# Kernel tuning notes

Hardware: AMD Instinct MI355X
Metric: run time of the kernel (lower is better)

The kernel has to match this reference:

```python
import jax, jax.numpy as jnp
import numpy as np

H = 16      # numHeads (== numKeyValueHeads since keyValueHeadsPerHead=1)
D = 128     # headDim


def setup_inputs() -> dict:
    key = jax.random.key(0)
    k1, k2, k3 = jax.random.split(key, 3)
    B, S, dim = 2, 2048, 2048
    x = jax.random.normal(k1, (B, S, dim), dtype=jnp.float32)
    # qkvProj: Linear(dim -> (H + 2*H)*D) without bias; torch Linear weight is [out, in]
    Wqkv = jax.random.normal(k2, ((H + 2 * H) * D, dim), dtype=jnp.float32) * 0.02
    # outProj: Linear(H*D -> dim) without bias
    Wout = jax.random.normal(k3, (dim, H * D), dtype=jnp.float32) * 0.02
    return {"x": x, "Wqkv": Wqkv, "Wout": Wout}


def reference(x, Wqkv, Wout):
    B, S, _ = x.shape
    qkv = jnp.einsum('bsd,ed->bse', x, Wqkv)           # [B, S, 3*H*D]
    qkv = qkv.reshape(B, S, 3 * H, D)
    q = qkv[:, :, :H]                                  # [B, S, H, D]
    k = qkv[:, :, H:2 * H]                             # [B, S, H, D]
    v = qkv[:, :, 2 * H:]                              # [B, S, H, D]
    # explicit QK^T / sqrt(d), softmax in fp32, then @ V (keyValueHeadsPerHead=1
    # collapses the group axis, leaving standard per-head attention)
    logits = jnp.einsum('bqhd,bkhd->bhqk', q, k) * (D ** -0.5)
    w = jax.nn.softmax(logits.astype(jnp.float32), axis=-1).astype(logits.dtype)
    out = jnp.einsum('bhqk,bkhd->bqhd', w, v).reshape(B, S, H * D)
    return jnp.einsum('bse,de->bsd', out, Wout)        # outProj
```

## Files before the change

kernel.cpp:

```cpp
#include <hip/hip_runtime.h>

typedef __bf16 bf16x8 __attribute__((ext_vector_type(8)));
typedef _Float16 f16;
typedef f16 f16x8 __attribute__((ext_vector_type(8)));
typedef float f32x4 __attribute__((ext_vector_type(4)));
typedef unsigned short u16;
typedef u16 u16x4 __attribute__((ext_vector_type(4)));

__device__ __forceinline__ u16 f2bf(float f) {
  unsigned u = __builtin_bit_cast(unsigned, f);
  u += 0x7FFFu + ((u >> 16) & 1u);
  return (u16)(u >> 16);
}

#define GLDS16(g, l) __builtin_amdgcn_global_load_lds(                     \
    (const __attribute__((address_space(1))) unsigned int*)(g),            \
    (__attribute__((address_space(3))) unsigned int*)(l), 16, 0, 0)

__device__ __forceinline__ f32x4 mfma16(bf16x8 a, bf16x8 b, f32x4 c) {
  return __builtin_amdgcn_mfma_f32_16x16x32_bf16(a, b, c, 0, 0, 0);
}
__device__ __forceinline__ f32x4 mfma16h(f16x8 a, f16x8 b, f32x4 c) {
  return __builtin_amdgcn_mfma_f32_16x16x32_f16(a, b, c, 0, 0, 0);
}

__global__ void cvt_bf16(const float* __restrict__ src, u16* __restrict__ dst,
                         int n4, int n4s, float scale) {
  int idx = blockIdx.x * blockDim.x + threadIdx.x;
  int stride = gridDim.x * blockDim.x;
  for (int i = idx; i < n4; i += stride) {
    float4 v = ((const float4*)src)[i];
    float sc = (i < n4s) ? scale : 1.0f;
    u16x4 o = { f2bf(v.x * sc), f2bf(v.y * sc), f2bf(v.z * sc), f2bf(v.w * sc) };
    ((u16x4*)dst)[i] = o;
  }
}

__global__ __launch_bounds__(512, 1) void gemm1_qkv(
    const u16* __restrict__ A, const u16* __restrict__ B,
    u16* __restrict__ QK, u16* __restrict__ VT) {
  __shared__ __align__(16) u16 LA[2][16384];
  __shared__ __align__(16) u16 LB[2][16384];
  constexpr int K = 2048;
  const int t = threadIdx.x, lane = t & 63, w = t >> 6;
  const int wm = w >> 2, wn = w & 3;
  const int l15 = lane & 15, lg = lane >> 4;
  const int l7 = l15 & 7;

  const int bid = blockIdx.x;
  const int wg = (bid & 7) * 48 + (bid >> 3);
  const int bx = wg % 24, by = wg / 24;
  const int m0 = by * 256, n0 = bx * 256;

  const int srow = t >> 3;
  const int schunk = (t & 7) ^ (srow & 7);
  const u16* ga = A + (size_t)(m0 + srow) * K + schunk * 8;
  const u16* gb = B + (size_t)(n0 + srow) * K + schunk * 8;

  f32x4 acc[8][4] = {};

#define STG_A(ch, kt, bfi)                                                 \
    GLDS16(ga + (kt) * 64 + (size_t)(ch) * 64 * K, &LA[bfi][(ch) * 4096] + t * 8)
#define STG_B(ch, kt, bfi)                                                 \
    GLDS16(gb + (kt) * 64 + (size_t)(ch) * 64 * K, &LB[bfi][(ch) * 4096] + t * 8)

  STG_A(0, 0, 0); STG_A(2, 0, 0);
  STG_B(0, 0, 0); STG_B(1, 0, 0); STG_B(2, 0, 0); STG_B(3, 0, 0);
  STG_A(1, 0, 0); STG_A(3, 0, 0);
  asm volatile("s_waitcnt vmcnt(2)" ::: "memory");
  __builtin_amdgcn_s_barrier();

#pragma unroll 1
  for (int T = 0; T < 32; ++T) {
    const int p = T & 1, np = p ^ 1;
    const bool st = (T < 31);
    const u16* la = &LA[p][0];
    const u16* lb = &LB[p][0];
    bf16x8 aF[2][4], bF0[2][2], bF1[2][2];

#pragma unroll
    for (int kk = 0; kk < 2; ++kk) {
      const int cp = ((kk * 4 + lg) ^ l7) * 8;
#pragma unroll
      for (int i = 0; i < 4; ++i)
        aF[kk][i] = *(const bf16x8*)&la[(wm * 128 + i * 16 + l15) * 64 + cp];
#pragma unroll
      for (int j = 0; j < 2; ++j)
        bF0[kk][j] = *(const bf16x8*)&lb[(wn * 64 + j * 16 + l15) * 64 + cp];
    }
    if (st) { STG_A(0, T + 1, np); STG_A(2, T + 1, np); }
    __builtin_amdgcn_s_barrier();
    asm volatile("s_waitcnt lgkmcnt(0)" ::: "memory");
    __builtin_amdgcn_sched_barrier(0);
    __builtin_amdgcn_s_setprio(1);
#pragma unroll
    for (int i = 0; i < 4; ++i)
#pragma unroll
      for (int j = 0; j < 2; ++j)
#pragma unroll
        for (int kk = 0; kk < 2; ++kk)
          acc[i][j] = mfma16(aF[kk][i], bF0[kk][j], acc[i][j]);
    __builtin_amdgcn_s_setprio(0);
    __builtin_amdgcn_s_barrier();

#pragma unroll
    for (int kk = 0; kk < 2; ++kk) {
      const int cp = ((kk * 4 + lg) ^ l7) * 8;
#pragma unroll
      for (int j = 0; j < 2; ++j)
        bF1[kk][j] = *(const bf16x8*)&lb[(wn * 64 + 32 + j * 16 + l15) * 64 + cp];
    }
    if (st) {
      STG_B(0, T + 1, np); STG_B(1, T + 1, np);
      asm volatile("s_waitcnt vmcnt(4)" ::: "memory");
    } else {
      asm volatile("s_waitcnt vmcnt(0)" ::: "memory");
    }
    __builtin_amdgcn_s_barrier();
    asm volatile("s_waitcnt lgkmcnt(0)" ::: "memory");
    __builtin_amdgcn_sched_barrier(0);
    __builtin_amdgcn_s_setprio(1);
#pragma unroll
    for (int i = 0; i < 4; ++i)
#pragma unroll
      for (int j = 0; j < 2; ++j)
#pragma unroll
        for (int kk = 0; kk < 2; ++kk)
          acc[i][2 + j] = mfma16(aF[kk][i], bF1[kk][j], acc[i][2 + j]);
    __builtin_amdgcn_s_setprio(0);
    __builtin_amdgcn_s_barrier();

#pragma unroll
    for (int kk = 0; kk < 2; ++kk) {
      const int cp = ((kk * 4 + lg) ^ l7) * 8;
#pragma unroll
      for (int i = 0; i < 4; ++i)
        aF[kk][i] = *(const bf16x8*)&la[(wm * 128 + 64 + i * 16 + l15) * 64 + cp];
    }
    if (st) { STG_B(2, T + 1, np); STG_B(3, T + 1, np); }
    __builtin_amdgcn_s_barrier();
    asm volatile("s_waitcnt lgkmcnt(0)" ::: "memory");
    __builtin_amdgcn_sched_barrier(0);
    __builtin_amdgcn_s_setprio(1);
#pragma unroll
    for (int i = 0; i < 4; ++i)
#pragma unroll
      for (int j = 0; j < 2; ++j)
#pragma unroll
        for (int kk = 0; kk < 2; ++kk)
          acc[4 + i][j] = mfma16(aF[kk][i], bF0[kk][j], acc[4 + i][j]);
    __builtin_amdgcn_s_setprio(0);
    __builtin_amdgcn_s_barrier();

    if (st) {
      STG_A(1, T + 1, np); STG_A(3, T + 1, np);
      asm volatile("s_waitcnt vmcnt(2)" ::: "memory");
    }
    __builtin_amdgcn_s_barrier();
    __builtin_amdgcn_s_setprio(1);
#pragma unroll
    for (int i = 0; i < 4; ++i)
#pragma unroll
      for (int j = 0; j < 2; ++j)
#pragma unroll
        for (int kk = 0; kk < 2; ++kk)
          acc[4 + i][2 + j] = mfma16(aF[kk][i], bF1[kk][j], acc[4 + i][2 + j]);
    __builtin_amdgcn_s_setprio(0);
    __builtin_amdgcn_s_barrier();
  }
#undef STG_A
#undef STG_B

  const int rb = m0 + wm * 128 + lg * 4;
  const int cb0 = wn * 64 + l15;
  if (n0 < 4096) {
#pragma unroll
    for (int i = 0; i < 8; ++i)
#pragma unroll
      for (int j = 0; j < 4; ++j) {
        const int row0 = rb + i * 16;
        const int col = n0 + cb0 + j * 16;
#pragma unroll
        for (int jj = 0; jj < 4; ++jj)
          QK[(size_t)(row0 + jj) * 4096 + col] = f2bf(acc[i][j][jj]);
      }
  } else {
#pragma unroll
    for (int i = 0; i < 8; ++i)
#pragma unroll
      for (int j = 0; j < 4; ++j) {
        const int row0 = rb + i * 16;
        const int vcol = (n0 - 4096) + cb0 + j * 16;
        const int bb = row0 >> 11, s = row0 & 2047;
        auto h0 = __builtin_amdgcn_cvt_pkrtz(acc[i][j][0], acc[i][j][1]);
        auto h1 = __builtin_amdgcn_cvt_pkrtz(acc[i][j][2], acc[i][j][3]);
        uint2 pk;
        pk.x = __builtin_bit_cast(unsigned, h0);
        pk.y = __builtin_bit_cast(unsigned, h1);
        *(uint2*)&VT[((size_t)bb * 2048 + vcol) * 2048 + s] = pk;
      }
  }
}

__global__ __launch_bounds__(256, 3) void gemm_bt(
    const u16* __restrict__ A, const u16* __restrict__ B,
    float* __restrict__ C, int M, int N, int K) {
  __shared__ __align__(16) u16 As[2][128 * 32];
  __shared__ __align__(16) u16 Bs[2][128 * 32];
  const int t = threadIdx.x;
  const int lane = t & 63;
  const int w = t >> 6;
  const int wm = w >> 1, wn = w & 1;
  const int l15 = lane & 15, lg = lane >> 4;
  const int m0 = blockIdx.y * 128, n0 = blockIdx.x * 128;
  f32x4 acc[4][4] = {};

  const int srow = t >> 2;
  const int schunk = (t & 3) ^ ((srow >> 1) & 3);
  const u16* ga = A + (size_t)(m0 + srow) * K + schunk * 8;
  const u16* gb = B + (size_t)(n0 + srow) * K + schunk * 8;
  const size_t half = (size_t)64 * K;
  const int ro = l15 * 32 + ((lg ^ ((l15 >> 1) & 3)) * 8);

#define STG(kt, bf) do {                                                   \
    const int ko_ = (kt) * 32;                                             \
    GLDS16(ga + ko_,        &As[bf][0] + t * 8);                           \
    GLDS16(ga + half + ko_, &As[bf][2048] + t * 8);                        \
    GLDS16(gb + ko_,        &Bs[bf][0] + t * 8);                           \
    GLDS16(gb + half + ko_, &Bs[bf][2048] + t * 8);                        \
  } while (0)

#define BODY(bf) do {                                                      \
    const u16* la_ = &As[bf][0];                                           \
    const u16* lb_ = &Bs[bf][0];                                           \
    bf16x8 af[4], bfr[4];                                                  \
    _Pragma("unroll")                                                      \
    for (int i_ = 0; i_ < 4; ++i_)                                         \
      af[i_] = *(const bf16x8*)&la_[(wm * 64 + i_ * 16) * 32 + ro];        \
    _Pragma("unroll")                                                      \
    for (int i_ = 0; i_ < 4; ++i_)                                         \
      bfr[i_] = *(const bf16x8*)&lb_[(wn * 64 + i_ * 16) * 32 + ro];       \
    __builtin_amdgcn_s_setprio(1);                                         \
    _Pragma("unroll")                                                      \
    for (int i_ = 0; i_ < 4; ++i_)                                         \
      _Pragma("unroll")                                                    \
      for (int j_ = 0; j_ < 4; ++j_)                                       \
        acc[i_][j_] = mfma16(af[i_], bfr[j_], acc[i_][j_]);                \
    __builtin_amdgcn_s_setprio(0);                                         \
  } while (0)

  const int NT = K / 32;
  STG(0, 0);
#pragma unroll 1
  for (int T = 0; T < NT - 1; ++T) {
    STG(T + 1, (T + 1) & 1);
    asm volatile("s_waitcnt vmcnt(4)" ::: "memory");
    __builtin_amdgcn_sched_barrier(0);
    __builtin_amdgcn_s_barrier();
    __builtin_amdgcn_sched_barrier(0);
    BODY(T & 1);
    asm volatile("s_waitcnt lgkmcnt(0)" ::: "memory");
    __builtin_amdgcn_sched_barrier(0);
    __builtin_amdgcn_s_barrier();
    __builtin_amdgcn_sched_barrier(0);
  }
  asm volatile("s_waitcnt vmcnt(0)" ::: "memory");
  __builtin_amdgcn_sched_barrier(0);
  __builtin_amdgcn_s_barrier();
  __builtin_amdgcn_sched_barrier(0);
  BODY((NT - 1) & 1);
#undef STG
#undef BODY

  const int rbase = m0 + wm * 64 + (lg << 2);
  const int cbase = n0 + wn * 64 + l15;
#pragma unroll
  for (int i = 0; i < 4; ++i)
#pragma unroll
    for (int j = 0; j < 4; ++j) {
      const int row0 = rbase + i * 16;
      const int col = cbase + j * 16;
#pragma unroll
      for (int jj = 0; jj < 4; ++jj)
        C[(size_t)(row0 + jj) * N + col] = acc[i][j][jj];
    }
}

#define PSTRIDE 72
__global__ __launch_bounds__(512, 1) void attn_fwd(
    const u16* __restrict__ qk, const u16* __restrict__ vt, u16* __restrict__ aout) {
  __shared__ __align__(16) u16 Ks[2][64 * 128];
  __shared__ __align__(16) u16 Vs[2][128 * 64];
  __shared__ __align__(16) u16 Pl[8][32 * PSTRIDE];
  const int t = threadIdx.x, lane = t & 63, w = t >> 6;
  const int bh = blockIdx.x;
  const int b = bh >> 4, h = bh & 15;
  const int q0 = blockIdx.y * 256 + w * 32;
  const int l15 = lane & 15, lg = lane >> 4;

  const u16* qp = qk + (size_t)b * 2048 * 4096 + h * 128;
  const u16* kp = qp + 2048;
  const u16* vtp = vt + (size_t)(b * 16 + h) * 128 * 2048;
  u16* op = aout + (size_t)b * 2048 * 2048 + h * 128;

  int ksoff[2], vsoff[2];
#pragma unroll
  for (int rd = 0; rd < 2; ++rd) {
    const int r = rd * 32 + (t >> 4);
    const int c = (t & 15) ^ (r & 15);
    ksoff[rd] = r * 4096 + c * 8;
    const int rv = rd * 64 + (t >> 3);
    const int cv = (t & 7) ^ (rv & 7);
    vsoff[rd] = rv * 2048 + cv * 8;
  }

  bf16x8 qf[2][4];
#pragma unroll
  for (int mi = 0; mi < 2; ++mi)
#pragma unroll
    for (int kd = 0; kd < 4; ++kd)
      qf[mi][kd] = *(const bf16x8*)&qp[(size_t)(q0 + mi * 16 + l15) * 4096 + kd * 32 + lg * 8];

  f32x4 o[2][8] = {};
  f32x4 lacc[2] = {};
  const f16x8 onesf = {f16(1.f), f16(1.f), f16(1.f), f16(1.f),
                       f16(1.f), f16(1.f), f16(1.f), f16(1.f)};
  u16* pw = &Pl[w][0];

#pragma unroll
  for (int rd = 0; rd < 2; ++rd) {
    GLDS16(kp + ksoff[rd], &Ks[0][0] + rd * 4096 + t * 8);
    GLDS16(vtp + vsoff[rd], &Vs[0][0] + rd * 4096 + t * 8);
  }
  __syncthreads();

  auto tile = [&](const u16* ksb, const u16* vsb, u16* kpre, u16* vpre, int nextit) {
    if (nextit < 32) {
      const size_t kt1 = (size_t)nextit * 64;
#pragma unroll
      for (int rd = 0; rd < 2; ++rd) {
        GLDS16(kp + kt1 * 4096 + ksoff[rd], kpre + rd * 4096 + t * 8);
        GLDS16(vtp + kt1 + vsoff[rd], vpre + rd * 4096 + t * 8);
      }
    }
    f32x4 sf[2][4];
    __builtin_amdgcn_s_setprio(1);
#pragma unroll
    for (int ni = 0; ni < 4; ++ni) {
      const int r = ni * 16 + l15;
      bf16x8 kf[4];
#pragma unroll
      for (int kd = 0; kd < 4; ++kd)
        kf[kd] = *(const bf16x8*)&ksb[r * 128 + (((kd * 4 + lg) ^ l15) * 8)];
#pragma unroll
      for (int mi = 0; mi < 2; ++mi) {
        f32x4 s = {0.f, 0.f, 0.f, 0.f};
        s = mfma16(kf[0], qf[mi][0], s);
        s = mfma16(kf[1], qf[mi][1], s);
        s = mfma16(kf[2], qf[mi][2], s);
        s = mfma16(kf[3], qf[mi][3], s);
        sf[mi][ni] = s;
      }
    }
    __builtin_amdgcn_s_setprio(0);

#pragma unroll
    for (int mi = 0; mi < 2; ++mi)
#pragma unroll
      for (int ni = 0; ni < 4; ++ni) {
        float p0 = exp2f(sf[mi][ni][0]);
        float p1 = exp2f(sf[mi][ni][1]);
        float p2 = exp2f(sf[mi][ni][2]);
        float p3 = exp2f(sf[mi][ni][3]);
        auto h0 = __builtin_amdgcn_cvt_pkrtz(p0, p1);
        auto h1 = __builtin_amdgcn_cvt_pkrtz(p2, p3);
        uint2 wv;
        wv.x = __builtin_bit_cast(unsigned, h0);
        wv.y = __builtin_bit_cast(unsigned, h1);
        *(uint2*)&pw[(mi * 16 + l15) * PSTRIDE + ni * 16 + lg * 4] = wv;
      }

    f16x8 pa[2][2];
#pragma unroll
    for (int mi = 0; mi < 2; ++mi)
#pragma unroll
      for (int ks = 0; ks < 2; ++ks)
        pa[mi][ks] = *(const f16x8*)&pw[(mi * 16 + l15) * PSTRIDE + ks * 32 + lg * 8];
    __builtin_amdgcn_s_setprio(1);
#pragma unroll
    for (int mi = 0; mi < 2; ++mi) {
      lacc[mi] = mfma16h(pa[mi][0], onesf, lacc[mi]);
      lacc[mi] = mfma16h(pa[mi][1], onesf, lacc[mi]);
    }
#pragma unroll
    for (int n2 = 0; n2 < 8; ++n2) {
      const int r = n2 * 16 + l15;
      f16x8 vf0 = *(const f16x8*)&vsb[r * 64 + (((0 * 4 + lg) ^ (l15 & 7)) * 8)];
      f16x8 vf1 = *(const f16x8*)&vsb[r * 64 + (((1 * 4 + lg) ^ (l15 & 7)) * 8)];
#pragma unroll
      for (int mi = 0; mi < 2; ++mi) {
        o[mi][n2] = mfma16h(pa[mi][0], vf0, o[mi][n2]);
        o[mi][n2] = mfma16h(pa[mi][1], vf1, o[mi][n2]);
      }
    }
    __builtin_amdgcn_s_setprio(0);
    __syncthreads();
  };

#pragma unroll 1
  for (int it = 0; it < 32; it += 2) {
    tile(&Ks[0][0], &Vs[0][0], &Ks[1][0], &Vs[1][0], it + 1);
    tile(&Ks[1][0], &Vs[1][0], &Ks[0][0], &Vs[0][0], it + 2);
  }

#pragma unroll
  for (int mi = 0; mi < 2; ++mi)
#pragma unroll
    for (int j = 0; j < 4; ++j) {
      float inv = 1.f / lacc[mi][j];
#pragma unroll
      for (int n2 = 0; n2 < 8; ++n2)
        op[(size_t)(q0 + mi * 16 + lg * 4 + j) * 2048 + n2 * 16 + l15] =
            f2bf(o[mi][n2][j] * inv);
    }
}

extern "C" void kernel_launch(void* const* d_in, const int* in_sizes, int n_in,
                              void* d_out, int out_size, void* d_ws, size_t ws_size,
                              hipStream_t stream) {
  const float* x    = (const float*)d_in[0];
  const float* Wqkv = (const float*)d_in[1];
  const float* Wout = (const float*)d_in[2];
  float* out = (float*)d_out;

  u16* ws = (u16*)d_ws;
  u16* xb    = ws;
  u16* wqkvb = ws + 8388608;
  u16* woutb = ws + 20971520;
  u16* qkbuf = ws + 25165824;
  u16* vtbuf = ws + 41943040;
  u16* aout  = xb;

  const float qscale = 0.08838834764831845f * 1.4426950408889634f;

  cvt_bf16<<<2048, 256, 0, stream>>>(x,    xb,    8388608 / 4, 0, 1.0f);
  cvt_bf16<<<2048, 256, 0, stream>>>(Wqkv, wqkvb, 12582912 / 4, 4194304 / 4, qscale);
  cvt_bf16<<<1024, 256, 0, stream>>>(Wout, woutb, 4194304 / 4, 0, 1.0f);

  gemm1_qkv<<<384, 512, 0, stream>>>(xb, wqkvb, qkbuf, vtbuf);
  attn_fwd<<<dim3(32, 8, 1), 512, 0, stream>>>(qkbuf, vtbuf, aout);
  gemm_bt<<<dim3(16, 32), 256, 0, stream>>>(aout, woutb, out, 4096, 2048, 2048);
}
```

Measured before the change: 272.2 us.

## Retile QKV GEMM to 128x192 blocks with two workgroups per CU

The QKV projection GEMM moves from 256x256 tiles with 512 threads, one block per CU and 384 blocks, to 128x192 tiles with 256 threads, two blocks per CU and 1024 blocks. The staging schedule, vmcnt waits and epilogue are reworked so a single tile can span both the QK and V column regions. The intent is better wave quantization across CUs and latency hiding through two resident blocks. The cost is lower data reuse per tile and more global/LDS traffic per FLOP.

```diff
diff --git a/kernel.cpp b/kernel.cpp
--- a/kernel.cpp
+++ b/kernel.cpp
@@ -36,38 +36,39 @@
   }
 }
 
-__global__ __launch_bounds__(512, 1) void gemm1_qkv(
+__global__ __launch_bounds__(256, 2) void gemm1_qkv(
     const u16* __restrict__ A, const u16* __restrict__ B,
     u16* __restrict__ QK, u16* __restrict__ VT) {
-  __shared__ __align__(16) u16 LA[2][16384];
-  __shared__ __align__(16) u16 LB[2][16384];
+  __shared__ __align__(16) u16 LA[2][8192];
+  __shared__ __align__(16) u16 LB[2][12288];
   constexpr int K = 2048;
   const int t = threadIdx.x, lane = t & 63, w = t >> 6;
-  const int wm = w >> 2, wn = w & 3;
+  const int wm = w >> 1, wn = w & 1;
   const int l15 = lane & 15, lg = lane >> 4;
   const int l7 = l15 & 7;
 
   const int bid = blockIdx.x;
-  const int wg = (bid & 7) * 48 + (bid >> 3);
-  const int bx = wg % 24, by = wg / 24;
-  const int m0 = by * 256, n0 = bx * 256;
+  const int wg = (bid & 7) * 128 + (bid >> 3);
+  const int bx = wg & 31, by = wg >> 5;
+  const int m0 = by * 128, n0 = bx * 192;
 
   const int srow = t >> 3;
   const int schunk = (t & 7) ^ (srow & 7);
   const u16* ga = A + (size_t)(m0 + srow) * K + schunk * 8;
   const u16* gb = B + (size_t)(n0 + srow) * K + schunk * 8;
 
-  f32x4 acc[8][4] = {};
+  f32x4 acc[4][6] = {};
 
 #define STG_A(ch, kt, bfi)                                                 \
-    GLDS16(ga + (kt) * 64 + (size_t)(ch) * 64 * K, &LA[bfi][(ch) * 4096] + t * 8)
+    GLDS16(ga + (kt) * 64 + (size_t)(ch) * 32 * K, &LA[bfi][(ch) * 2048] + t * 8)
 #define STG_B(ch, kt, bfi)                                                 \
-    GLDS16(gb + (kt) * 64 + (size_t)(ch) * 64 * K, &LB[bfi][(ch) * 4096] + t * 8)
-
-  STG_A(0, 0, 0); STG_A(2, 0, 0);
-  STG_B(0, 0, 0); STG_B(1, 0, 0); STG_B(2, 0, 0); STG_B(3, 0, 0);
+    GLDS16(gb + (kt) * 64 + (size_t)(ch) * 32 * K, &LB[bfi][(ch) * 2048] + t * 8)
+
+  STG_A(0, 0, 0); STG_A(2, 0, 0); STG_B(0, 0, 0);
+  STG_B(1, 0, 0); STG_B(3, 0, 0); STG_B(4, 0, 0);
+  STG_B(2, 0, 0); STG_B(5, 0, 0);
   STG_A(1, 0, 0); STG_A(3, 0, 0);
-  asm volatile("s_waitcnt vmcnt(2)" ::: "memory");
+  asm volatile("s_waitcnt vmcnt(4)" ::: "memory");
   __builtin_amdgcn_s_barrier();
 
 #pragma unroll 1
@@ -76,30 +77,35 @@
     const bool st = (T < 31);
     const u16* la = &LA[p][0];
     const u16* lb = &LB[p][0];
-    bf16x8 aF[2][4], bF0[2][2], bF1[2][2];
+    bf16x8 aF[2][2], bLo[2][3], bHi[2][3];
 
 #pragma unroll
     for (int kk = 0; kk < 2; ++kk) {
       const int cp = ((kk * 4 + lg) ^ l7) * 8;
 #pragma unroll
-      for (int i = 0; i < 4; ++i)
-        aF[kk][i] = *(const bf16x8*)&la[(wm * 128 + i * 16 + l15) * 64 + cp];
-#pragma unroll
-      for (int j = 0; j < 2; ++j)
-        bF0[kk][j] = *(const bf16x8*)&lb[(wn * 64 + j * 16 + l15) * 64 + cp];
-    }
-    if (st) { STG_A(0, T + 1, np); STG_A(2, T + 1, np); }
+      for (int i = 0; i < 2; ++i)
+        aF[kk][i] = *(const bf16x8*)&la[(wm * 64 + i * 16 + l15) * 64 + cp];
+#pragma unroll
+      for (int j = 0; j < 3; ++j)
+        bLo[kk][j] = *(const bf16x8*)&lb[(wn * 96 + j * 16 + l15) * 64 + cp];
+    }
+    if (st) {
+      STG_A(0, T + 1, np); STG_A(2, T + 1, np); STG_B(0, T + 1, np);
+      asm volatile("s_waitcnt vmcnt(5)" ::: "memory");
+    } else {
+      asm volatile("s_waitcnt vmcnt(2)" ::: "memory");
+    }
     __builtin_amdgcn_s_barrier();
     asm volatile("s_waitcnt lgkmcnt(0)" ::: "memory");
     __builtin_amdgcn_sched_barrier(0);
     __builtin_amdgcn_s_setprio(1);
 #pragma unroll
-    for (int i = 0; i < 4; ++i)
-#pragma unroll
-      for (int j = 0; j < 2; ++j)
+    for (int i = 0; i < 2; ++i)
+#pragma unroll
+      for (int j = 0; j < 3; ++j)
 #pragma unroll
         for (int kk = 0; kk < 2; ++kk)
-          acc[i][j] = mfma16(aF[kk][i], bF0[kk][j], acc[i][j]);
+          acc[i][j] = mfma16(aF[kk][i], bLo[kk][j], acc[i][j]);
     __builtin_amdgcn_s_setprio(0);
     __builtin_amdgcn_s_barrier();
 
@@ -107,12 +113,12 @@
     for (int kk = 0; kk < 2; ++kk) {
       const int cp = ((kk * 4 + lg) ^ l7) * 8;
 #pragma unroll
-      for (int j = 0; j < 2; ++j)
-        bF1[kk][j] = *(const bf16x8*)&lb[(wn * 64 + 32 + j * 16 + l15) * 64 + cp];
+      for (int j = 0; j < 3; ++j)
+        bHi[kk][j] = *(const bf16x8*)&lb[(wn * 96 + 48 + j * 16 + l15) * 64 + cp];
     }
     if (st) {
-      STG_B(0, T + 1, np); STG_B(1, T + 1, np);
-      asm volatile("s_waitcnt vmcnt(4)" ::: "memory");
+      STG_B(1, T + 1, np); STG_B(3, T + 1, np); STG_B(4, T + 1, np);
+      asm volatile("s_waitcnt vmcnt(6)" ::: "memory");
     } else {
       asm volatile("s_waitcnt vmcnt(0)" ::: "memory");
     }
@@ -121,12 +127,12 @@
     __builtin_amdgcn_sched_barrier(0);
     __builtin_amdgcn_s_setprio(1);
 #pragma unroll
-    for (int i = 0; i < 4; ++i)
-#pragma unroll
-      for (int j = 0; j < 2; ++j)
+    for (int i = 0; i < 2; ++i)
+#pragma unroll
+      for (int j = 0; j < 3; ++j)
 #pragma unroll
         for (int kk = 0; kk < 2; ++kk)
-          acc[i][2 + j] = mfma16(aF[kk][i], bF1[kk][j], acc[i][2 + j]);
+          acc[i][3 + j] = mfma16(aF[kk][i], bHi[kk][j], acc[i][3 + j]);
     __builtin_amdgcn_s_setprio(0);
     __builtin_amdgcn_s_barrier();
 
@@ -134,63 +140,57 @@
     for (int kk = 0; kk < 2; ++kk) {
       const int cp = ((kk * 4 + lg) ^ l7) * 8;
 #pragma unroll
-      for (int i = 0; i < 4; ++i)
-        aF[kk][i] = *(const bf16x8*)&la[(wm * 128 + 64 + i * 16 + l15) * 64 + cp];
-    }
-    if (st) { STG_B(2, T + 1, np); STG_B(3, T + 1, np); }
+      for (int i = 0; i < 2; ++i)
+        aF[kk][i] = *(const bf16x8*)&la[(wm * 64 + 32 + i * 16 + l15) * 64 + cp];
+    }
+    if (st) { STG_B(2, T + 1, np); STG_B(5, T + 1, np); }
     __builtin_amdgcn_s_barrier();
     asm volatile("s_waitcnt lgkmcnt(0)" ::: "memory");
     __builtin_amdgcn_sched_barrier(0);
     __builtin_amdgcn_s_setprio(1);
 #pragma unroll
-    for (int i = 0; i < 4; ++i)
-#pragma unroll
-      for (int j = 0; j < 2; ++j)
+    for (int i = 0; i < 2; ++i)
+#pragma unroll
+      for (int j = 0; j < 3; ++j)
 #pragma unroll
         for (int kk = 0; kk < 2; ++kk)
-          acc[4 + i][j] = mfma16(aF[kk][i], bF0[kk][j], acc[4 + i][j]);
+          acc[2 + i][j] = mfma16(aF[kk][i], bLo[kk][j], acc[2 + i][j]);
     __builtin_amdgcn_s_setprio(0);
     __builtin_amdgcn_s_barrier();
 
     if (st) {
       STG_A(1, T + 1, np); STG_A(3, T + 1, np);
-      asm volatile("s_waitcnt vmcnt(2)" ::: "memory");
-    }
-    __builtin_amdgcn_s_barrier();
-    __builtin_amdgcn_s_setprio(1);
-#pragma unroll
-    for (int i = 0; i < 4; ++i)
-#pragma unroll
-      for (int j = 0; j < 2; ++j)
+      asm volatile("s_waitcnt vmcnt(4)" ::: "memory");
+    }
+    __builtin_amdgcn_s_barrier();
+    __builtin_amdgcn_s_setprio(1);
+#pragma unroll
+    for (int i = 0; i < 2; ++i)
+#pragma unroll
+      for (int j = 0; j < 3; ++j)
 #pragma unroll
         for (int kk = 0; kk < 2; ++kk)
-          acc[4 + i][2 + j] = mfma16(aF[kk][i], bF1[kk][j], acc[4 + i][2 + j]);
+          acc[2 + i][3 + j] = mfma16(aF[kk][i], bHi[kk][j], acc[2 + i][3 + j]);
     __builtin_amdgcn_s_setprio(0);
     __builtin_amdgcn_s_barrier();
   }
 #undef STG_A
 #undef STG_B
 
-  const int rb = m0 + wm * 128 + lg * 4;
-  const int cb0 = wn * 64 + l15;
-  if (n0 < 4096) {
-#pragma unroll
-    for (int i = 0; i < 8; ++i)
-#pragma unroll
-      for (int j = 0; j < 4; ++j) {
-        const int row0 = rb + i * 16;
-        const int col = n0 + cb0 + j * 16;
+  const int rb = m0 + wm * 64 + lg * 4;
+  const int cb = n0 + wn * 96 + l15;
+#pragma unroll
+  for (int i = 0; i < 4; ++i) {
+#pragma unroll
+    for (int j = 0; j < 6; ++j) {
+      const int row0 = rb + i * 16;
+      const int col = cb + j * 16;
+      if (col < 4096) {
 #pragma unroll
         for (int jj = 0; jj < 4; ++jj)
           QK[(size_t)(row0 + jj) * 4096 + col] = f2bf(acc[i][j][jj]);
-      }
-  } else {
-#pragma unroll
-    for (int i = 0; i < 8; ++i)
-#pragma unroll
-      for (int j = 0; j < 4; ++j) {
-        const int row0 = rb + i * 16;
-        const int vcol = (n0 - 4096) + cb0 + j * 16;
+      } else {
+        const int vcol = col - 4096;
         const int bb = row0 >> 11, s = row0 & 2047;
         auto h0 = __builtin_amdgcn_cvt_pkrtz(acc[i][j][0], acc[i][j][1]);
         auto h1 = __builtin_amdgcn_cvt_pkrtz(acc[i][j][2], acc[i][j][3]);
@@ -199,6 +199,7 @@
         pk.y = __builtin_bit_cast(unsigned, h1);
         *(uint2*)&VT[((size_t)bb * 2048 + vcol) * 2048 + s] = pk;
       }
+    }
   }
 }
 
@@ -447,7 +448,7 @@
   cvt_bf16<<<2048, 256, 0, stream>>>(Wqkv, wqkvb, 12582912 / 4, 4194304 / 4, qscale);
   cvt_bf16<<<1024, 256, 0, stream>>>(Wout, woutb, 4194304 / 4, 0, 1.0f);
 
-  gemm1_qkv<<<384, 512, 0, stream>>>(xb, wqkvb, qkbuf, vtbuf);
+  gemm1_qkv<<<1024, 256, 0, stream>>>(xb, wqkvb, qkbuf, vtbuf);
   attn_fwd<<<dim3(32, 8, 1), 512, 0, stream>>>(qkbuf, vtbuf, aout);
   gemm_bt<<<dim3(16, 32), 256, 0, stream>>>(aout, woutb, out, 4096, 2048, 2048);
 }
```

Measured after the change: 259.1 us. 1.05x faster.
